# Performance work log

Measured on AMD Instinct MI355X. Metric: run time of the kernel, lower is better.

The kernel has to match this reference:

```python
import jax, jax.numpy as jnp
import numpy as np

G = 32          # grid_size
H = 12          # num_heads
D = 768         # embed_dim
HD = D // H     # head_dim = 64
FF = 3072       # ff_dim
B, T = 2, 2048
SPAN = 2 * G - 1        # 63
SPAN_C = 4 * G + 1      # 129
EPS = 1e-5


def setup_inputs() -> dict:
    key = jax.random.key(0)
    ks = jax.random.split(key, 16)
    s = 0.02
    is_sep = jax.random.uniform(ks[6], (T,)) < 0.05
    demo_id = jax.random.randint(ks[5], (T,), 0, 8)
    demo_id = jnp.where(is_sep, -1, demo_id)
    return {
        'x': jax.random.normal(ks[0], (B, T, D), jnp.float32),
        'row': jax.random.randint(ks[1], (T,), 0, G),
        'col': jax.random.randint(ks[2], (T,), 0, G),
        'demo_row': jax.random.randint(ks[3], (T,), 0, G),
        'demo_col': jax.random.randint(ks[4], (T,), 0, 2 * G),
        'demo_id': demo_id,
        'is_sep': is_sep,
        'ln1_w': jnp.ones((D,), jnp.float32),
        'ln1_b': jnp.zeros((D,), jnp.float32),
        'ln2_w': jnp.ones((D,), jnp.float32),
        'ln2_b': jnp.zeros((D,), jnp.float32),
        'qkv_w': jax.random.normal(ks[7], (D, 3 * D), jnp.float32) * s,
        'qkv_b': jnp.zeros((3 * D,), jnp.float32),
        'proj_w': jax.random.normal(ks[8], (D, D), jnp.float32) * s,
        'proj_b': jnp.zeros((D,), jnp.float32),
        'ff1_w': jax.random.normal(ks[9], (D, FF), jnp.float32) * s,
        'ff1_b': jnp.zeros((FF,), jnp.float32),
        'ff2_w': jax.random.normal(ks[10], (FF, D), jnp.float32) * s,
        'ff2_b': jnp.zeros((D,), jnp.float32),
        'rel_emb': jax.random.normal(ks[11], (SPAN * SPAN, H), jnp.float32) * s,
        'demo_emb': jax.random.normal(ks[12], (SPAN_C * SPAN, H), jnp.float32) * s,
    }


def _ln(x, w, b):
    m = jnp.mean(x, -1, keepdims=True)
    v = jnp.mean((x - m) ** 2, -1, keepdims=True)
    return (x - m) / jnp.sqrt(v + EPS) * w + b


def _rel_bias(rel_emb, row, col, is_sep):
    g1 = G - 1
    dr = jnp.clip(row[:, None] - row[None, :], -g1, g1) + g1
    dc = jnp.clip(col[:, None] - col[None, :], -g1, g1) + g1
    bias = rel_emb[dr * SPAN + dc]              # (T, T, H)
    valid = ~is_sep
    vp = (valid[:, None] & valid[None, :]).astype(jnp.float32)
    return jnp.transpose(bias, (2, 0, 1)) * vp[None]  # (H, T, T)


def _demo_bias(demo_emb, drow, dcol, did, is_sep):
    g1 = G - 1
    dr = jnp.clip(drow[:, None] - drow[None, :], -g1, g1) + g1
    dc = jnp.clip(dcol[:, None] - dcol[None, :], -2 * G, 2 * G) + 2 * G
    bias = demo_emb[dr * SPAN_C + dc]           # (T, T, H)
    valid = ~is_sep
    same = (did[:, None] == did[None, :]) & (did[:, None] >= 0) & (did[None, :] >= 0)
    vp = (valid[:, None] & valid[None, :] & same).astype(jnp.float32)
    return jnp.transpose(bias, (2, 0, 1)) * vp[None]


def reference(x, row, col, demo_row, demo_col, demo_id, is_sep,
              ln1_w, ln1_b, ln2_w, ln2_b, qkv_w, qkv_b, proj_w, proj_b,
              ff1_w, ff1_b, ff2_w, ff2_b, rel_emb, demo_emb):
    b, t, d = x.shape
    h1 = _ln(x, ln1_w, ln1_b)
    qkv = h1 @ qkv_w + qkv_b                        # (B, T, 3D)
    q, k, v = jnp.split(qkv, 3, axis=-1)
    q = q.reshape(b, t, H, HD).transpose(0, 2, 1, 3)  # (B, H, T, HD)
    k = k.reshape(b, t, H, HD).transpose(0, 2, 1, 3)
    v = v.reshape(b, t, H, HD).transpose(0, 2, 1, 3)
    scale = float(HD) ** -0.5
    logits = jnp.einsum('bhqd,bhkd->bhqk', q, k) * scale
    bias = _rel_bias(rel_emb, row, col, is_sep) + _demo_bias(demo_emb, demo_row, demo_col, demo_id, is_sep)
    attn = jax.nn.softmax(logits + bias[None], axis=-1)
    out = jnp.einsum('bhqk,bhkd->bhqd', attn, v)
    out = out.transpose(0, 2, 1, 3).reshape(b, t, D)
    out = out @ proj_w + proj_b
    x = x + out
    h2 = _ln(x, ln2_w, ln2_b)
    ff = jax.nn.gelu(h2 @ ff1_w + ff1_b, approximate=False) @ ff2_w + ff2_b
    return x + ff
```

## Files before the change

### kernel.cpp

```cpp
#include <hip/hip_runtime.h>
#include <hip/hip_bf16.h>
#include <math.h>

#define G_ 32
#define H_ 12
#define D_ 768
#define HD_ 64
#define FF_ 3072
#define B_ 2
#define T_ 2048
#define SPAN_ 63
#define SPANC_ 129
#define EPSF 1e-5f

typedef short bf16x8 __attribute__((ext_vector_type(8)));
typedef short short4v __attribute__((ext_vector_type(4)));
typedef float f32x4 __attribute__((ext_vector_type(4)));

__device__ __forceinline__ short f2bf(float f) {
    unsigned u = __builtin_bit_cast(unsigned, f);
    u = u + 0x7FFFu + ((u >> 16) & 1u);
    return (short)(u >> 16);
}

__global__ __launch_bounds__(256) void ln_bf16_kernel(const float* __restrict__ x,
                                                      const float* __restrict__ w,
                                                      const float* __restrict__ b,
                                                      short* __restrict__ out) {
    int wv = threadIdx.x >> 6;
    int lane = threadIdx.x & 63;
    int rowi = blockIdx.x * 4 + wv;
    const float* xr = x + (size_t)rowi * D_;
    float vals[12];
    float s = 0.f;
#pragma unroll
    for (int i = 0; i < 12; ++i) { vals[i] = xr[lane + i * 64]; s += vals[i]; }
#pragma unroll
    for (int off = 32; off > 0; off >>= 1) s += __shfl_xor(s, off, 64);
    float mean = s * (1.0f / D_);
    float vs = 0.f;
#pragma unroll
    for (int i = 0; i < 12; ++i) { float d = vals[i] - mean; vs += d * d; }
#pragma unroll
    for (int off = 32; off > 0; off >>= 1) vs += __shfl_xor(vs, off, 64);
    float rstd = rsqrtf(vs * (1.0f / D_) + EPSF);
    short* outr = out + (size_t)rowi * D_;
#pragma unroll
    for (int i = 0; i < 12; ++i) {
        int c = lane + i * 64;
        outr[c] = f2bf((vals[i] - mean) * rstd * w[c] + b[c]);
    }
}

__global__ __launch_bounds__(256) void tcast_kernel(const float* __restrict__ W,
                                                    short* __restrict__ Wt,
                                                    int K, int N) {
    __shared__ float t[32][33];
    int n0 = blockIdx.x * 32, k0 = blockIdx.y * 32;
    int tid = threadIdx.x;
    int r = tid >> 3, c4 = (tid & 7) * 4;
    float4 v = *(const float4*)(W + (size_t)(k0 + r) * N + n0 + c4);
    t[r][c4 + 0] = v.x; t[r][c4 + 1] = v.y; t[r][c4 + 2] = v.z; t[r][c4 + 3] = v.w;
    __syncthreads();
    short4v o;
    o[0] = f2bf(t[c4 + 0][r]); o[1] = f2bf(t[c4 + 1][r]);
    o[2] = f2bf(t[c4 + 2][r]); o[3] = f2bf(t[c4 + 3][r]);
    *(short4v*)(Wt + (size_t)(n0 + r) * K + k0 + c4) = o;
}

__global__ __launch_bounds__(256) void bias_build(
    const int* __restrict__ rowp, const int* __restrict__ colp,
    const int* __restrict__ drowp, const int* __restrict__ dcolp,
    const int* __restrict__ didp,
    const float* __restrict__ rel_emb, const float* __restrict__ demo_emb,
    ushort* __restrict__ biasT) {
    __shared__ ushort patch[12][16][72];
    int k0 = blockIdx.x * 64, q0 = blockIdx.y * 16;
    int tid = threadIdx.x;
    int qi = tid >> 4, kq = (tid & 15) * 4;
    int q = q0 + qi;
    int idq = didp[q];
    int rq = rowp[q], cq = colp[q], drq = drowp[q], dcq = dcolp[q];
#pragma unroll
    for (int j = 0; j < 4; ++j) {
        int k = k0 + kq + j;
        int idk = didp[k];
        float4 v0 = {0.f, 0.f, 0.f, 0.f}, v1 = v0, v2 = v0;
        if (idq >= 0 && idk >= 0) {
            int dr = min(max(rq - rowp[k], -(G_ - 1)), G_ - 1) + (G_ - 1);
            int dc = min(max(cq - colp[k], -(G_ - 1)), G_ - 1) + (G_ - 1);
            const float* rp = rel_emb + (size_t)(dr * SPAN_ + dc) * 12;
            v0 = *(const float4*)rp;
            v1 = *(const float4*)(rp + 4);
            v2 = *(const float4*)(rp + 8);
            if (idq == idk) {
                int ddr = min(max(drq - drowp[k], -(G_ - 1)), G_ - 1) + (G_ - 1);
                int ddc = min(max(dcq - dcolp[k], -2 * G_), 2 * G_) + 2 * G_;
                const float* dp = demo_emb + (size_t)(ddr * SPANC_ + ddc) * 12;
                float4 w0 = *(const float4*)dp;
                float4 w1 = *(const float4*)(dp + 4);
                float4 w2 = *(const float4*)(dp + 8);
                v0.x += w0.x; v0.y += w0.y; v0.z += w0.z; v0.w += w0.w;
                v1.x += w1.x; v1.y += w1.y; v1.z += w1.z; v1.w += w1.w;
                v2.x += w2.x; v2.y += w2.y; v2.z += w2.z; v2.w += w2.w;
            }
        }
        float bv[12] = {v0.x, v0.y, v0.z, v0.w, v1.x, v1.y, v1.z, v1.w,
                        v2.x, v2.y, v2.z, v2.w};
        int kl = kq + j;
#pragma unroll
        for (int h = 0; h < 12; ++h) patch[h][qi][kl] = (ushort)f2bf(bv[h]);
    }
    __syncthreads();
    for (int c = tid; c < 1536; c += 256) {
        int rowid = c >> 3, off = (c & 7) * 8;
        int h = rowid >> 4, q2 = rowid & 15;
        *(bf16x8*)(biasT + (size_t)h * T_ * T_ + (size_t)(q0 + q2) * T_ + k0 + off) =
            *(const bf16x8*)&patch[h][q2][off];
    }
}

enum { EPI_NONE = 0, EPI_RES = 1, EPI_GELU = 2 };

template <int EPI, int BF16OUT>
__global__ __launch_bounds__(256, 2) void gemm_bf16(const short* __restrict__ A,
                                                    const short* __restrict__ Bt,
                                                    const float* __restrict__ bias,
                                                    const float* __restrict__ res,
                                                    void* __restrict__ Cv,
                                                    int M, int N, int K) {
    __shared__ short As[128 * 64];
    __shared__ short Bs[128 * 64];
    int tid = threadIdx.x;
    int l = tid & 63;
    int w = tid >> 6;
    int wm = w >> 1, wn = w & 1;
    int row0 = blockIdx.y * 128, col0 = blockIdx.x * 128;
    int g = l >> 4, c16 = l & 15;
    f32x4 zero = {0.f, 0.f, 0.f, 0.f};
    f32x4 acc[4][4];
#pragma unroll
    for (int m = 0; m < 4; ++m)
#pragma unroll
        for (int n = 0; n < 4; ++n) acc[m][n] = zero;

    for (int k0 = 0; k0 < K; k0 += 64) {
#pragma unroll
        for (int p = 0; p < 4; ++p) {
            int sidx = p * 256 + tid;
            int row = sidx >> 3, cseg = sidx & 7;
            int ds = row * 64 + ((cseg ^ (row & 7)) << 3);
            *(bf16x8*)&As[ds] = *(const bf16x8*)(A + (size_t)(row0 + row) * K + k0 + cseg * 8);
            *(bf16x8*)&Bs[ds] = *(const bf16x8*)(Bt + (size_t)(col0 + row) * K + k0 + cseg * 8);
        }
        __syncthreads();
#pragma unroll
        for (int dk = 0; dk < 2; ++dk) {
            bf16x8 af[4], bfr[4];
#pragma unroll
            for (int m = 0; m < 4; ++m) {
                int r = wm * 64 + m * 16 + c16;
                af[m] = *(const bf16x8*)&As[r * 64 + (((dk * 4 + g) ^ (r & 7)) << 3)];
            }
#pragma unroll
            for (int n = 0; n < 4; ++n) {
                int r = wn * 64 + n * 16 + c16;
                bfr[n] = *(const bf16x8*)&Bs[r * 64 + (((dk * 4 + g) ^ (r & 7)) << 3)];
            }
#pragma unroll
            for (int m = 0; m < 4; ++m)
#pragma unroll
                for (int n = 0; n < 4; ++n)
                    acc[m][n] = __builtin_amdgcn_mfma_f32_16x16x32_bf16(af[m], bfr[n], acc[m][n], 0, 0, 0);
        }
        __syncthreads();
    }

#pragma unroll
    for (int m = 0; m < 4; ++m)
#pragma unroll
        for (int n = 0; n < 4; ++n) {
            int rrow = row0 + wm * 64 + m * 16 + g * 4;
            int ccol = col0 + wn * 64 + n * 16 + c16;
            float bv = bias[ccol];
#pragma unroll
            for (int i = 0; i < 4; ++i) {
                float v = acc[m][n][i] + bv;
                if (EPI == EPI_GELU) v = 0.5f * v * (1.f + erff(v * 0.70710678118f));
                if (EPI == EPI_RES) v += res[(size_t)(rrow + i) * N + ccol];
                if (BF16OUT)
                    ((short*)Cv)[(size_t)(rrow + i) * N + ccol] = f2bf(v);
                else
                    ((float*)Cv)[(size_t)(rrow + i) * N + ccol] = v;
            }
        }
}

__global__ __launch_bounds__(256, 2) void attn_mfma(
    const short* __restrict__ qkv,
    const ushort* __restrict__ biasT,
    short* __restrict__ attn_o) {
    __shared__ short Ks[64 * 64];
    __shared__ short Vt[64 * 72];
    __shared__ short Pb[4][16 * 72];

    int tid = threadIdx.x, w = tid >> 6, l = tid & 63;
    int g = l >> 4, c16 = l & 15;
    int qt = blockIdx.x & 31, bh = blockIdx.x >> 5;
    int h = bh % H_, b = bh / H_;
    int q0 = qt * 64;
    const int QS = 3 * D_;
    const short* kvbase = qkv + (size_t)b * T_ * QS;

    bf16x8 qf[2];
    {
        int qrow = q0 + w * 16 + c16;
        const short* qp = kvbase + (size_t)qrow * QS + h * HD_;
#pragma unroll
        for (int dk = 0; dk < 2; ++dk) qf[dk] = *(const bf16x8*)(qp + dk * 32 + g * 8);
    }
    const ushort* bptr[4];
#pragma unroll
    for (int i = 0; i < 4; ++i)
        bptr[i] = biasT + (size_t)h * T_ * T_ + (size_t)(q0 + w * 16 + g * 4 + i) * T_;

    f32x4 zero = {0.f, 0.f, 0.f, 0.f};
    f32x4 oacc[4];
#pragma unroll
    for (int nf = 0; nf < 4; ++nf) oacc[nf] = zero;
    float lsum[4] = {0.f, 0.f, 0.f, 0.f};

    for (int kb = 0; kb < T_; kb += 64) {
        float bv[16];
#pragma unroll
        for (int nf = 0; nf < 4; ++nf)
#pragma unroll
            for (int i = 0; i < 4; ++i) {
                unsigned u = bptr[i][kb + nf * 16 + c16];
                bv[nf * 4 + i] = __builtin_bit_cast(float, u << 16);
            }
#pragma unroll
        for (int p = 0; p < 2; ++p) {
            int sidx = p * 256 + tid;
            int row = sidx >> 3, cseg = sidx & 7;
            *(bf16x8*)&Ks[row * 64 + ((cseg ^ (row & 7)) << 3)] =
                *(const bf16x8*)(kvbase + (size_t)(kb + row) * QS + D_ + h * HD_ + cseg * 8);
        }
        {
            int vrow = tid >> 2, part = tid & 3;
            const short* vp = kvbase + (size_t)(kb + vrow) * QS + 2 * D_ + h * HD_ + part * 16;
            bf16x8 v0 = *(const bf16x8*)(vp);
            bf16x8 v1 = *(const bf16x8*)(vp + 8);
            int kchunk = vrow >> 3, kpos = vrow & 7;
#pragma unroll
            for (int j = 0; j < 8; ++j) {
                int d = part * 16 + j;
                Vt[d * 72 + (((kchunk ^ (d >> 3)) & 7) << 3) + kpos] = v0[j];
            }
#pragma unroll
            for (int j = 0; j < 8; ++j) {
                int d = part * 16 + 8 + j;
                Vt[d * 72 + (((kchunk ^ (d >> 3)) & 7) << 3) + kpos] = v1[j];
            }
        }
        __syncthreads();

        f32x4 sac[4];
#pragma unroll
        for (int nf = 0; nf < 4; ++nf) sac[nf] = zero;
#pragma unroll
        for (int dk = 0; dk < 2; ++dk) {
#pragma unroll
            for (int nf = 0; nf < 4; ++nf) {
                int r = nf * 16 + c16;
                bf16x8 kf = *(const bf16x8*)&Ks[r * 64 + (((dk * 4 + g) ^ (r & 7)) << 3)];
                sac[nf] = __builtin_amdgcn_mfma_f32_16x16x32_bf16(qf[dk], kf, sac[nf], 0, 0, 0);
            }
        }

        float pp[4][4];
#pragma unroll
        for (int nf = 0; nf < 4; ++nf)
#pragma unroll
            for (int i = 0; i < 4; ++i) {
                float e = __expf(fmaf(sac[nf][i], 0.125f, bv[nf * 4 + i]));
                pp[nf][i] = e;
                lsum[i] += e;
            }
        short* pbw = &Pb[w][0];
#pragma unroll
        for (int nf = 0; nf < 4; ++nf) {
            int chunkbase = nf * 2 + (c16 >> 3);
            int kpos = c16 & 7;
#pragma unroll
            for (int i = 0; i < 4; ++i)
                pbw[(g * 4 + i) * 72 + (((chunkbase ^ g) & 7) << 3) + kpos] = f2bf(pp[nf][i]);
        }
#pragma unroll
        for (int dk = 0; dk < 2; ++dk) {
            bf16x8 pa = *(const bf16x8*)&pbw[c16 * 72 + (((dk * 4 + g) ^ (c16 >> 2)) & 7) * 8];
#pragma unroll
            for (int nf = 0; nf < 4; ++nf) {
                int d = nf * 16 + c16;
                bf16x8 vb = *(const bf16x8*)&Vt[d * 72 + (((dk * 4 + g) ^ (d >> 3)) & 7) * 8];
                oacc[nf] = __builtin_amdgcn_mfma_f32_16x16x32_bf16(pa, vb, oacc[nf], 0, 0, 0);
            }
        }
        __syncthreads();
    }

#pragma unroll
    for (int i = 0; i < 4; ++i) {
#pragma unroll
        for (int off = 1; off < 16; off <<= 1) lsum[i] += __shfl_xor(lsum[i], off, 64);
    }

#pragma unroll
    for (int nf = 0; nf < 4; ++nf)
#pragma unroll
        for (int i = 0; i < 4; ++i) {
            float o = oacc[nf][i] / lsum[i];
            int qq = q0 + w * 16 + g * 4 + i;
            attn_o[(size_t)(b * T_ + qq) * D_ + h * HD_ + nf * 16 + c16] = f2bf(o);
        }
}

extern "C" void kernel_launch(void* const* d_in, const int* in_sizes, int n_in,
                              void* d_out, int out_size, void* d_ws, size_t ws_size,
                              hipStream_t stream) {
    const float* x = (const float*)d_in[0];
    const int* rowp = (const int*)d_in[1];
    const int* colp = (const int*)d_in[2];
    const int* drowp = (const int*)d_in[3];
    const int* dcolp = (const int*)d_in[4];
    const int* didp = (const int*)d_in[5];
    const float* ln1_w = (const float*)d_in[7];
    const float* ln1_b = (const float*)d_in[8];
    const float* ln2_w = (const float*)d_in[9];
    const float* ln2_b = (const float*)d_in[10];
    const float* qkv_w = (const float*)d_in[11];
    const float* qkv_b = (const float*)d_in[12];
    const float* proj_w = (const float*)d_in[13];
    const float* proj_b = (const float*)d_in[14];
    const float* ff1_w = (const float*)d_in[15];
    const float* ff1_b = (const float*)d_in[16];
    const float* ff2_w = (const float*)d_in[17];
    const float* ff2_b = (const float*)d_in[18];
    const float* rel_emb = (const float*)d_in[19];
    const float* demo_emb = (const float*)d_in[20];
    float* out = (float*)d_out;

    const int M = B_ * T_;
    char* p = (char*)d_ws;
    short* h1 = (short*)p;     p += (size_t)M * D_ * 2;
    short* qkvb = (short*)p;   p += (size_t)M * 3 * D_ * 2;
    short* attn_o = (short*)p; p += (size_t)M * D_ * 2;
    short* qkvt = (short*)p;   p += (size_t)(3 * D_) * D_ * 2;
    short* projt = (short*)p;  p += (size_t)D_ * D_ * 2;
    short* ff1t = (short*)p;   p += (size_t)FF_ * D_ * 2;
    short* ff2t = (short*)p;   p += (size_t)D_ * FF_ * 2;
    float* x2 = (float*)p;
    short* h2 = (short*)(p + (size_t)M * D_ * 4);
    short* ffact = (short*)(p + (size_t)M * D_ * 4 + (size_t)M * D_ * 2);
    ushort* biasT = (ushort*)p;

    bias_build<<<dim3(T_ / 64, T_ / 16), 256, 0, stream>>>(
        rowp, colp, drowp, dcolp, didp, rel_emb, demo_emb, biasT);
    tcast_kernel<<<dim3(3 * D_ / 32, D_ / 32), 256, 0, stream>>>(qkv_w, qkvt, D_, 3 * D_);
    tcast_kernel<<<dim3(D_ / 32, D_ / 32), 256, 0, stream>>>(proj_w, projt, D_, D_);
    tcast_kernel<<<dim3(FF_ / 32, D_ / 32), 256, 0, stream>>>(ff1_w, ff1t, D_, FF_);
    tcast_kernel<<<dim3(D_ / 32, FF_ / 32), 256, 0, stream>>>(ff2_w, ff2t, FF_, D_);

    ln_bf16_kernel<<<dim3(M / 4), 256, 0, stream>>>(x, ln1_w, ln1_b, h1);

    gemm_bf16<EPI_NONE, 1><<<dim3(3 * D_ / 128, M / 128), 256, 0, stream>>>(
        h1, qkvt, qkv_b, nullptr, qkvb, M, 3 * D_, D_);

    attn_mfma<<<dim3(B_ * H_ * (T_ / 64)), 256, 0, stream>>>(qkvb, biasT, attn_o);

    gemm_bf16<EPI_RES, 0><<<dim3(D_ / 128, M / 128), 256, 0, stream>>>(
        attn_o, projt, proj_b, x, x2, M, D_, D_);

    ln_bf16_kernel<<<dim3(M / 4), 256, 0, stream>>>(x2, ln2_w, ln2_b, h2);

    gemm_bf16<EPI_GELU, 1><<<dim3(FF_ / 128, M / 128), 256, 0, stream>>>(
        h2, ff1t, ff1_b, nullptr, ffact, M, FF_, D_);

    gemm_bf16<EPI_RES, 0><<<dim3(D_ / 128, M / 128), 256, 0, stream>>>(
        ffact, ff2t, ff2_b, x2, out, M, D_, FF_);
}
```

Measured before the change: 277.1 us.

## Use direct global-to-LDS loads in GEMM and prefetch attention bias tiles

The GEMM tile staging now uses global_load_lds, so tiles go straight from global memory into LDS without passing through registers. The swizzle moves to the source address because the LDS destination is contiguous per wave. The attention kernel now loads next iteration's bias values one step ahead, a register double-buffer that hides their global latency behind the MFMA work. The risks are higher register pressure in attention and correctness depending on the per-lane LDS placement matching the XOR swizzle that the fragment reads expect.

```diff
diff --git a/kernel.cpp b/kernel.cpp
--- a/kernel.cpp
+++ b/kernel.cpp
@@ -21,6 +21,12 @@
     unsigned u = __builtin_bit_cast(unsigned, f);
     u = u + 0x7FFFu + ((u >> 16) & 1u);
     return (short)(u >> 16);
+}
+
+__device__ __forceinline__ void gl_lds16(const void* g, void* l) {
+    __builtin_amdgcn_global_load_lds(
+        (const __attribute__((address_space(1))) unsigned int*)g,
+        (__attribute__((address_space(3))) unsigned int*)l, 16, 0, 0);
 }
 
 __global__ __launch_bounds__(256) void ln_bf16_kernel(const float* __restrict__ x,
@@ -144,14 +150,18 @@
 #pragma unroll
         for (int n = 0; n < 4; ++n) acc[m][n] = zero;
 
+    int srow = w * 32 + (l >> 3);
+    int sseg0 = (l & 7);
+
     for (int k0 = 0; k0 < K; k0 += 64) {
 #pragma unroll
-        for (int p = 0; p < 4; ++p) {
-            int sidx = p * 256 + tid;
-            int row = sidx >> 3, cseg = sidx & 7;
-            int ds = row * 64 + ((cseg ^ (row & 7)) << 3);
-            *(bf16x8*)&As[ds] = *(const bf16x8*)(A + (size_t)(row0 + row) * K + k0 + cseg * 8);
-            *(bf16x8*)&Bs[ds] = *(const bf16x8*)(Bt + (size_t)(col0 + row) * K + k0 + cseg * 8);
+        for (int inst = 0; inst < 4; ++inst) {
+            int arow = srow + inst * 8;
+            int seg = sseg0 ^ (arow & 7);
+            gl_lds16(A + (size_t)(row0 + arow) * K + k0 + seg * 8,
+                     &As[(w * 32 + inst * 8) * 64]);
+            gl_lds16(Bt + (size_t)(col0 + arow) * K + k0 + seg * 8,
+                     &Bs[(w * 32 + inst * 8) * 64]);
         }
         __syncthreads();
 #pragma unroll
@@ -230,15 +240,23 @@
     for (int nf = 0; nf < 4; ++nf) oacc[nf] = zero;
     float lsum[4] = {0.f, 0.f, 0.f, 0.f};
 
+    unsigned bvu[16];
+#pragma unroll
+    for (int nf = 0; nf < 4; ++nf)
+#pragma unroll
+        for (int i = 0; i < 4; ++i)
+            bvu[nf * 4 + i] = bptr[i][nf * 16 + c16];
+
     for (int kb = 0; kb < T_; kb += 64) {
-        float bv[16];
-#pragma unroll
-        for (int nf = 0; nf < 4; ++nf)
-#pragma unroll
-            for (int i = 0; i < 4; ++i) {
-                unsigned u = bptr[i][kb + nf * 16 + c16];
-                bv[nf * 4 + i] = __builtin_bit_cast(float, u << 16);
-            }
+        unsigned bvn[16];
+        {
+            int kbn = (kb + 64) & (T_ - 1);
+#pragma unroll
+            for (int nf = 0; nf < 4; ++nf)
+#pragma unroll
+                for (int i = 0; i < 4; ++i)
+                    bvn[nf * 4 + i] = bptr[i][kbn + nf * 16 + c16];
+        }
 #pragma unroll
         for (int p = 0; p < 2; ++p) {
             int sidx = p * 256 + tid;
@@ -283,7 +301,8 @@
         for (int nf = 0; nf < 4; ++nf)
 #pragma unroll
             for (int i = 0; i < 4; ++i) {
-                float e = __expf(fmaf(sac[nf][i], 0.125f, bv[nf * 4 + i]));
+                float bvf = __builtin_bit_cast(float, bvu[nf * 4 + i] << 16);
+                float e = __expf(fmaf(sac[nf][i], 0.125f, bvf));
                 pp[nf][i] = e;
                 lsum[i] += e;
             }
@@ -306,6 +325,8 @@
                 oacc[nf] = __builtin_amdgcn_mfma_f32_16x16x32_bf16(pa, vb, oacc[nf], 0, 0, 0);
             }
         }
+#pragma unroll
+        for (int j = 0; j < 16; ++j) bvu[j] = bvn[j];
         __syncthreads();
     }
 
```

Measured after the change: 266.6 us. 1.04x faster.
